# Kernel optimization log

Measured on AMD Instinct MI355X. Metric: run time of the kernel, lower is better.

The kernel has to match this reference:

```python
import jax, jax.numpy as jnp
import numpy as np

B, C, H, W = 4, 64, 256, 256
DS = 4        # ClusterLocalAtt downscale
CS = 2        # FastClusterAtt cluster_stride
NH = 4        # FastClusterAtt num_heads
G = 4         # OrthoConvClustering groups
N_NOISE = 8   # number of -1 (noise) labels; even and divisible by B


def _maxpool(x, k):
    b, c, h, w = x.shape
    return x.reshape(b, c, h // k, k, w // k, k).max(axis=(3, 5))


def _normalize(x, eps=1e-12):
    n = jnp.linalg.norm(x, axis=-1, keepdims=True)
    return x / jnp.maximum(n, eps)


def _feat_sim(cf, nf):
    # cf: (B,k,HW), nf: (B,n,HW) -> (B,k) mean cosine similarity over noise rows
    return jnp.einsum('bkl,bnl->bkn', _normalize(cf), _normalize(nf)).mean(-1)


def setup_inputs():
    key = jax.random.key(0)
    ks = jax.random.split(key, 12)
    x = jax.random.normal(ks[0], (B, C, H, W), jnp.float32)
    noise_idx = jnp.arange(N_NOISE, dtype=jnp.int32)
    labels = jax.random.randint(ks[1], (B * C,), 0, 12, dtype=jnp.int32)
    labels = labels.at[noise_idx].set(-1)
    inv = 1.0 / np.sqrt(C // G)
    return {
        'x': x, 'labels': labels, 'noise_idx': noise_idx,
        'qkv_w1': jax.random.normal(ks[2], (3 * C,), jnp.float32) * 0.5,
        'qkv_b1': jax.random.normal(ks[3], (3 * C,), jnp.float32) * 0.1,
        'up_k': jax.random.normal(ks[4], (C, DS, DS), jnp.float32) * 0.25,
        'up_b': jax.random.normal(ks[5], (C,), jnp.float32) * 0.1,
        'clu_w': jax.random.normal(ks[6], (G, C // G, C // G), jnp.float32) * inv,
        'clu_b': jnp.zeros((C,), jnp.float32),
        'qkv_w2': jax.random.normal(ks[7], (3 * C,), jnp.float32) * 0.5,
        'bais_w': jax.random.normal(ks[8], (C, C), jnp.float32) * (inv * 0.5),
        'bais_b': jax.random.normal(ks[9], (C,), jnp.float32) * 0.1,
    }


def reference(x, labels, noise_idx, qkv_w1, qkv_b1, up_k, up_b,
              clu_w, clu_b, qkv_w2, bais_w, bais_b):
    idx3 = jnp.arange(3 * C) // 3  # grouped 1x1 conv (groups=C): out ch j reads in ch j//3
    # ================= ClusterLocalAtt =================
    x_down = _maxpool(x, DS)                        # (B,C,Hd,Wd)
    Hd, Wd = H // DS, W // DS
    hw = Hd * Wd
    qkv = x_down[:, idx3] * qkv_w1[None, :, None, None] + qkv_b1[None, :, None, None]
    qkv = qkv.reshape(3 * B * C, hw)                # torch: reshape(1, 3*B*C, hw)
    q, k, v = jnp.split(qkv, 3, axis=0)             # each (B*C, hw) - batch/ch mixed, faithful
    valid = labels != -1
    allowed = (labels[:, None] == labels[None, :]) & valid[:, None] & valid[None, :]
    scores = q @ k.T                                # (BC, BC)
    attn = jax.nn.softmax(jnp.where(allowed, scores, -1e30), axis=-1)
    att = jnp.where(valid[:, None], attn @ v, 0.0)  # noise rows stay zero
    out = att.reshape(B, C, Hd, Wd)
    # depthwise ConvTranspose2d(kernel=DS, stride=DS): each input px -> DSxDS block
    up = jnp.einsum('bchw,cpq->bchpwq', out, up_k).reshape(B, C, H, W)
    up = up + up_b[None, :, None, None]
    noise = x.reshape(B * C, H * W)[noise_idx].reshape(B, N_NOISE // B, H * W)
    sim = _feat_sim(up.reshape(B, C, H * W), noise)[:, :, None, None]  # (B,C,1,1)
    out_clu = x + (up + (1.0 - sim) * x)
    # ================= FastClusterAtt =================
    xf = out_clu.reshape(B, G, C // G, H * W)
    xc = jnp.einsum('goi,bgil->bgol', clu_w, xf).reshape(B, C, H * W) + clu_b[None, :, None]
    x_ds = _maxpool(xc.reshape(B, C, H, W), CS)     # (B,C,Hs,Ws)
    Hs, Ws = H // CS, W // CS
    Ls = Hs * Ws
    qkv2 = (x_ds[:, idx3] * qkv_w2[None, :, None, None]).reshape(B, 3, NH, C // NH, Ls)
    qh, kh, vh = qkv2[:, 0], qkv2[:, 1], qkv2[:, 2]  # (B,NH,hd,Ls)
    sc = (qh * kh).sum(axis=2, keepdims=True) / np.sqrt(C // NH)  # (B,NH,1,Ls)
    a = jax.nn.softmax(sc, axis=-1)
    oh = (a * vh).sum(axis=-1).reshape(B, C)        # (B,C) global pooled heads
    # bilinear upsample of a spatially-constant map is the same constant -> skip interp
    ov = jnp.einsum('oc,bc->bo', bais_w, oh) + bais_b
    out_full = jnp.broadcast_to(ov[:, :, None, None], (B, C, H, W))
    sim2 = _feat_sim(out_full.reshape(B, C, H * W), noise)[:, :, None, None]
    WWT = jnp.einsum('goi,gpi->gop', clu_w, clu_w)
    I = jnp.eye(C // G, dtype=clu_w.dtype)
    ortho = 1.0 - jax.lax.stop_gradient(jnp.mean((WWT - I) ** 2))
    out2 = out_full * (1.0 - sim2) + ortho * out_clu
    return out_clu + out2
```

## Files before the change

### kernel.cpp

```cpp
#include <hip/hip_runtime.h>
#include <math.h>

#define WS_XD     0u
#define WS_S      1048576u
#define WS_GPART  1048832u
#define WS_COEF   2113792u
#define WS_CONST  2138368u
#define WS_ATT    2138624u
#define WS_FAC    3187200u
#define WS_XDS    3187456u
#define WS_ALPHA  7382016u
#define WS_BETA   7382272u
#define WS_NSTAT  7382273u
#define WS_P2     7382304u

__device__ __forceinline__ float bsum(float v, float* sd, int tid) {
    sd[tid] = v; __syncthreads();
    for (int off = 128; off > 0; off >>= 1) {
        if (tid < off) sd[tid] += sd[tid + off];
        __syncthreads();
    }
    float r = sd[0]; __syncthreads(); return r;
}
__device__ __forceinline__ float bmax(float v, float* sd, int tid) {
    sd[tid] = v; __syncthreads();
    for (int off = 128; off > 0; off >>= 1) {
        if (tid < off) sd[tid] = fmaxf(sd[tid], sd[tid + off]);
        __syncthreads();
    }
    float r = sd[0]; __syncthreads(); return r;
}

__global__ __launch_bounds__(256) void k_pool4(const float* __restrict__ x,
                                               const int* __restrict__ nidx,
                                               float* __restrict__ ws) {
    __shared__ float sd[256];
    int r = blockIdx.x, tid = threadIdx.x;
    const float4* xr = (const float4*)x + (size_t)r * 16384;
    float* xd = ws + WS_XD + (size_t)r * 4096;
    float sum = 0.f, s = 0.f, ss = 0.f;
    for (int it = 0; it < 16; ++it) {
        int o = it * 256 + tid;
        int h = o >> 6, w = o & 63;
        float m = -INFINITY;
        #pragma unroll
        for (int p = 0; p < 4; ++p) {
            float4 v = xr[(4 * h + p) * 64 + w];
            m = fmaxf(m, fmaxf(fmaxf(v.x, v.y), fmaxf(v.z, v.w)));
            s  += v.x + v.y + v.z + v.w;
            ss += v.x*v.x + v.y*v.y + v.z*v.z + v.w*v.w;
        }
        xd[o] = m; sum += m;
    }
    float st = bsum(sum, sd, tid);
    if (tid == 0) ws[WS_S + r] = st;
    bool isn = false;
    #pragma unroll
    for (int n = 0; n < 8; ++n) isn = isn || (nidx[n] == r);
    if (isn) {
        float ts = bsum(s, sd, tid);
        float tss = bsum(ss, sd, tid);
        if (tid == 0) {
            for (int n = 0; n < 8; ++n)
                if (nidx[n] == r) { ws[WS_NSTAT + n] = ts; ws[WS_NSTAT + 8 + n] = sqrtf(tss); }
        }
    }
}

__global__ __launch_bounds__(256) void k_gram(float* __restrict__ ws) {
    __shared__ __align__(16) float As[64][68];
    __shared__ __align__(16) float Bs[64][68];
    int tid = threadIdx.x, tx = tid & 15, ty = tid >> 4;
    int ra0 = blockIdx.y * 64, rb0 = 80 + blockIdx.x * 64, k0 = blockIdx.z * 64;
    const float4* xd4 = (const float4*)(ws + WS_XD);
    #pragma unroll
    for (int q = 0; q < 4; ++q) {
        int idx = q * 256 + tid;
        int row = idx >> 4, cf = idx & 15;
        float4 a = xd4[(size_t)(ra0 + row) * 1024 + (k0 >> 2) + cf];
        As[cf*4+0][row] = a.x; As[cf*4+1][row] = a.y; As[cf*4+2][row] = a.z; As[cf*4+3][row] = a.w;
        float4 b = xd4[(size_t)(rb0 + row) * 1024 + (k0 >> 2) + cf];
        Bs[cf*4+0][row] = b.x; Bs[cf*4+1][row] = b.y; Bs[cf*4+2][row] = b.z; Bs[cf*4+3][row] = b.w;
    }
    __syncthreads();
    float acc[4][4] = {};
    #pragma unroll 4
    for (int kk = 0; kk < 64; ++kk) {
        float4 a = *(const float4*)&As[kk][ty * 4];
        float4 b = *(const float4*)&Bs[kk][tx * 4];
        acc[0][0] += a.x*b.x; acc[0][1] += a.x*b.y; acc[0][2] += a.x*b.z; acc[0][3] += a.x*b.w;
        acc[1][0] += a.y*b.x; acc[1][1] += a.y*b.y; acc[1][2] += a.y*b.z; acc[1][3] += a.y*b.w;
        acc[2][0] += a.z*b.x; acc[2][1] += a.z*b.y; acc[2][2] += a.z*b.z; acc[2][3] += a.z*b.w;
        acc[3][0] += a.w*b.x; acc[3][1] += a.w*b.y; acc[3][2] += a.w*b.z; acc[3][3] += a.w*b.w;
    }
    float* gp = ws + WS_GPART + (size_t)blockIdx.z * 16384;
    #pragma unroll
    for (int i = 0; i < 4; ++i) {
        float4 o = make_float4(acc[i][0], acc[i][1], acc[i][2], acc[i][3]);
        *(float4*)&gp[(size_t)(ra0 + ty * 4 + i) * 128 + blockIdx.x * 64 + tx * 4] = o;
    }
}

__global__ __launch_bounds__(256) void k_attn1(const int* __restrict__ labels,
                                               const float* __restrict__ w1,
                                               const float* __restrict__ b1,
                                               float* __restrict__ ws) {
    __shared__ float sd[256];
    __shared__ float attn_s[256];
    __shared__ float grow[128];
    int i = blockIdx.x, tid = threadIdx.x;
    int labi = labels[i];
    bool validi = (labi != -1);
    int bi = (i >= 192) ? 1 : 0;
    int ji = i - bi * 192;
    int rq = bi * 64 + ji / 3;
    if (tid < 128) {
        const float* gp = ws + WS_GPART + (size_t)rq * 128 + tid;
        float acc = 0.f;
        #pragma unroll 8
        for (int p = 0; p < 64; ++p) acc += gp[(size_t)p * 16384];
        grow[tid] = acc;
    }
    __syncthreads();
    float wq = w1[ji], bq = b1[ji];
    int gk = 256 + tid;
    int bk = (gk >= 384) ? 2 : 1;
    int jk = gk - bk * 192;
    int rk = bk * 64 + jk / 3;
    float wk = w1[jk], bbk = b1[jk];
    int labj = labels[tid];
    bool allowed = validi && (labj == labi) && (labj != -1);
    float score = wq * wk * grow[rk - 80]
                + wq * bbk * ws[WS_S + rq]
                + wk * bq  * ws[WS_S + rk]
                + 4096.0f * bq * bbk;
    float sc = allowed ? score : -1e30f;
    float m = bmax(sc, sd, tid);
    float e = __expf(sc - m);
    float Z = bsum(e, sd, tid);
    float attn = validi ? (e / Z) : 0.0f;
    attn_s[tid] = attn;
    int gv = 512 + tid;
    int bv = (gv >= 576) ? 3 : 2;
    int jv = gv - bv * 192;
    float csum = bsum(attn * b1[jv], sd, tid);
    if (tid < 96) {
        float s = 0.0f;
        if (tid < 86) {
            int rv = 170 + tid;
            int lo, hi, jadd;
            if (rv < 192) { int c = rv - 128; lo = 3 * c; if (lo < 128) lo = 128; hi = 3 * c + 2; jadd = -128; }
            else          { int c = rv - 192; lo = 3 * c; hi = 3 * c + 2; jadd = 64; }
            for (int jj = lo; jj <= hi; ++jj) s += attn_s[jj + jadd] * w1[jj];
        }
        ws[WS_COEF + i * 96 + tid] = s;
    }
    if (tid == 0) ws[WS_CONST + i] = csum;
}

__global__ __launch_bounds__(256) void k_attmm(float* __restrict__ ws) {
    __shared__ __align__(16) float As[96][68];
    __shared__ __align__(16) float Bs[96][64];
    int tid = threadIdx.x, tx = tid & 15, ty = tid >> 4;
    int col0 = blockIdx.x * 64, row0 = blockIdx.y * 64;
    const float4* cf4 = (const float4*)(ws + WS_COEF);
    const float4* xd4 = (const float4*)(ws + WS_XD);
    #pragma unroll
    for (int q = 0; q < 6; ++q) {
        int f = q * 256 + tid;
        {
            int row = f / 24, c24 = f - row * 24;
            float4 v = cf4[(size_t)(row0 + row) * 24 + c24];
            As[c24*4+0][row] = v.x; As[c24*4+1][row] = v.y; As[c24*4+2][row] = v.z; As[c24*4+3][row] = v.w;
        }
        {
            int row = f >> 4, c16 = f & 15;
            float4 v = make_float4(0.f, 0.f, 0.f, 0.f);
            if (row < 86) v = xd4[(size_t)(170 + row) * 1024 + (col0 >> 2) + c16];
            *(float4*)&Bs[row][c16 * 4] = v;
        }
    }
    __syncthreads();
    float acc[4][4] = {};
    #pragma unroll 4
    for (int kk = 0; kk < 96; ++kk) {
        float4 a = *(const float4*)&As[kk][ty * 4];
        float4 b = *(const float4*)&Bs[kk][tx * 4];
        acc[0][0] += a.x*b.x; acc[0][1] += a.x*b.y; acc[0][2] += a.x*b.z; acc[0][3] += a.x*b.w;
        acc[1][0] += a.y*b.x; acc[1][1] += a.y*b.y; acc[1][2] += a.y*b.z; acc[1][3] += a.y*b.w;
        acc[2][0] += a.z*b.x; acc[2][1] += a.z*b.y; acc[2][2] += a.z*b.z; acc[2][3] += a.z*b.w;
        acc[3][0] += a.w*b.x; acc[3][1] += a.w*b.y; acc[3][2] += a.w*b.z; acc[3][3] += a.w*b.w;
    }
    float* att = ws + WS_ATT;
    #pragma unroll
    for (int i = 0; i < 4; ++i) {
        int row = row0 + ty * 4 + i;
        float cv = ws[WS_CONST + row];
        float4 o = make_float4(acc[i][0] + cv, acc[i][1] + cv, acc[i][2] + cv, acc[i][3] + cv);
        *(float4*)&att[(size_t)row * 4096 + col0 + tx * 4] = o;
    }
}

__global__ __launch_bounds__(256) void k_sim(const float* __restrict__ x,
                                             const int* __restrict__ nidx,
                                             const float* __restrict__ upk,
                                             const float* __restrict__ upb,
                                             float* __restrict__ ws) {
    __shared__ float sd[256];
    int r = blockIdx.x, tid = threadIdx.x;
    int b = r >> 6, c = r & 63;
    const float* att = ws + WS_ATT + (size_t)r * 4096;
    const float4* xn0 = (const float4*)x + (size_t)nidx[2 * b] * 16384;
    const float4* xn1 = (const float4*)x + (size_t)nidx[2 * b + 1] * 16384;
    const float4* k4p = (const float4*)upk + c * 4;
    float ub = upb[c];
    float4 kk0 = k4p[0], kk1 = k4p[1], kk2 = k4p[2], kk3 = k4p[3];
    float s2 = 0.f, d0 = 0.f, d1 = 0.f;
    for (int it = 0; it < 64; ++it) {
        int f = it * 256 + tid;
        int rowf = f >> 6, c4 = f & 63;
        float av = att[(rowf >> 2) * 64 + c4];
        int p = rowf & 3;
        float4 kv = (p == 0) ? kk0 : ((p == 1) ? kk1 : ((p == 2) ? kk2 : kk3));
        float4 a0 = xn0[f], a1 = xn1[f];
        float u;
        u = av * kv.x + ub; s2 += u * u; d0 += u * a0.x; d1 += u * a1.x;
        u = av * kv.y + ub; s2 += u * u; d0 += u * a0.y; d1 += u * a1.y;
        u = av * kv.z + ub; s2 += u * u; d0 += u * a0.z; d1 += u * a1.z;
        u = av * kv.w + ub; s2 += u * u; d0 += u * a0.w; d1 += u * a1.w;
    }
    s2 = bsum(s2, sd, tid);
    d0 = bsum(d0, sd, tid);
    d1 = bsum(d1, sd, tid);
    if (tid == 0) {
        float nup = fmaxf(sqrtf(s2), 1e-12f);
        float n0 = fmaxf(ws[WS_NSTAT + 8 + 2 * b], 1e-12f);
        float n1 = fmaxf(ws[WS_NSTAT + 8 + 2 * b + 1], 1e-12f);
        float sim = 0.5f * (d0 / (nup * n0) + d1 / (nup * n1));
        ws[WS_FAC + r] = 2.0f - sim;
    }
}

__global__ __launch_bounds__(128) void k_cluds(const float* __restrict__ x,
                                               const float* __restrict__ upk,
                                               const float* __restrict__ upb,
                                               const float* __restrict__ cw,
                                               const float* __restrict__ cb,
                                               float* __restrict__ ws) {
    __shared__ float wcl[256];
    __shared__ float kup[256];
    __shared__ float cbl[16], ubl[16], fcl[16];
    int h2 = blockIdx.x, g = blockIdx.y, b = blockIdx.z;
    int t = threadIdx.x;
    wcl[t] = cw[g * 256 + t];       wcl[t + 128] = cw[g * 256 + t + 128];
    kup[t] = upk[g * 256 + t];      kup[t + 128] = upk[g * 256 + t + 128];
    if (t < 16) {
        cbl[t] = cb[g * 16 + t];
        ubl[t] = upb[g * 16 + t];
        fcl[t] = ws[WS_FAC + b * 64 + g * 16 + t];
    }
    __syncthreads();
    int r0 = 2 * h2;
    int p0 = r0 & 3;
    int q0 = (2 * t) & 3;
    int h_att = h2 >> 1;
    int wa = t >> 1;
    const float* attb = ws + WS_ATT;
    float oc[16][4];
    #pragma unroll
    for (int i = 0; i < 16; ++i) {
        int ch = g * 16 + i;
        float av = attb[(size_t)(b * 64 + ch) * 4096 + h_att * 64 + wa];
        const float* xc = x + (size_t)(b * 64 + ch) * 65536;
        float2 x0 = *(const float2*)&xc[r0 * 256 + 2 * t];
        float2 x1 = *(const float2*)&xc[(r0 + 1) * 256 + 2 * t];
        float ub = ubl[i], fc = fcl[i];
        oc[i][0] = av * kup[i * 16 + p0 * 4 + q0]           + ub + fc * x0.x;
        oc[i][1] = av * kup[i * 16 + p0 * 4 + q0 + 1]       + ub + fc * x0.y;
        oc[i][2] = av * kup[i * 16 + (p0 + 1) * 4 + q0]     + ub + fc * x1.x;
        oc[i][3] = av * kup[i * 16 + (p0 + 1) * 4 + q0 + 1] + ub + fc * x1.y;
    }
    float* xds = ws + WS_XDS;
    #pragma unroll
    for (int o = 0; o < 16; ++o) {
        float cbv = cbl[o];
        float a0 = cbv, a1 = cbv, a2 = cbv, a3 = cbv;
        #pragma unroll
        for (int i = 0; i < 16; ++i) {
            float wv = wcl[o * 16 + i];
            a0 += wv * oc[i][0]; a1 += wv * oc[i][1];
            a2 += wv * oc[i][2]; a3 += wv * oc[i][3];
        }
        float m = fmaxf(fmaxf(a0, a1), fmaxf(a2, a3));
        xds[(size_t)((b * 64 + g * 16 + o) * 128 + h2) * 128 + t] = m;
    }
}

__global__ __launch_bounds__(256) void k_attn2a(const float* __restrict__ w2,
                                                float* __restrict__ ws) {
    __shared__ float wl2[192];
    __shared__ float ms[256], dsh[256];
    __shared__ float ns[256][17];
    int chunk = blockIdx.x, nh = blockIdx.y, b = blockIdx.z, tid = threadIdx.x;
    if (tid < 192) wl2[tid] = w2[tid];
    __syncthreads();
    const float4* X4 = (const float4*)(ws + WS_XDS + (size_t)b * 1048576);
    int li = chunk * 256 + tid;
    float4 sc = make_float4(0.f, 0.f, 0.f, 0.f);
    #pragma unroll
    for (int d = 0; d < 16; ++d) {
        int jq = nh * 16 + d, jk = 64 + nh * 16 + d;
        float4 q4 = X4[(size_t)(jq / 3) * 4096 + li];
        float4 k4 = X4[(size_t)(jk / 3) * 4096 + li];
        float wqk = wl2[jq] * wl2[jk] * 0.25f;
        sc.x += wqk * q4.x * k4.x; sc.y += wqk * q4.y * k4.y;
        sc.z += wqk * q4.z * k4.z; sc.w += wqk * q4.w * k4.w;
    }
    float m = fmaxf(fmaxf(sc.x, sc.y), fmaxf(sc.z, sc.w));
    float p0 = __expf(sc.x - m), p1 = __expf(sc.y - m), p2 = __expf(sc.z - m), p3 = __expf(sc.w - m);
    float den = p0 + p1 + p2 + p3;
    float num[16];
    #pragma unroll
    for (int d = 0; d < 16; ++d) {
        int jv = 128 + nh * 16 + d;
        float4 v4 = X4[(size_t)(jv / 3) * 4096 + li];
        num[d] = wl2[jv] * (p0 * v4.x + p1 * v4.y + p2 * v4.z + p3 * v4.w);
    }
    ms[tid] = m; dsh[tid] = den;
    #pragma unroll
    for (int d = 0; d < 16; ++d) ns[tid][d] = num[d];
    __syncthreads();
    for (int off = 128; off > 0; off >>= 1) {
        if (tid < off) {
            float ma = ms[tid], mb = ms[tid + off];
            float M = fmaxf(ma, mb);
            float ra = __expf(ma - M), rb = __expf(mb - M);
            dsh[tid] = dsh[tid] * ra + dsh[tid + off] * rb;
            #pragma unroll
            for (int d = 0; d < 16; ++d)
                ns[tid][d] = ns[tid][d] * ra + ns[tid + off][d] * rb;
            ms[tid] = M;
        }
        __syncthreads();
    }
    if (tid == 0) {
        float* p = ws + WS_P2 + ((size_t)(b * 4 + nh) * 16 + chunk) * 18;
        p[0] = ms[0]; p[1] = dsh[0];
        #pragma unroll
        for (int d = 0; d < 16; ++d) p[2 + d] = ns[0][d];
    }
}

__global__ __launch_bounds__(256) void k_tail(const float* __restrict__ bw,
                                              const float* __restrict__ bb,
                                              const float* __restrict__ cw,
                                              float* __restrict__ ws) {
    __shared__ float ohs[256], sd[256];
    int tid = threadIdx.x;
    int grp = tid >> 4;
    int j = tid & 15;
    const float* p = ws + WS_P2 + ((size_t)grp * 16 + j) * 18;
    float m = p[0], den = p[1], num[16];
    #pragma unroll
    for (int d = 0; d < 16; ++d) num[d] = p[2 + d];
    #pragma unroll
    for (int mask = 1; mask <= 8; mask <<= 1) {
        float mo = __shfl_xor(m, mask);
        float dn = __shfl_xor(den, mask);
        float M = fmaxf(m, mo);
        float ra = __expf(m - M), rb = __expf(mo - M);
        den = den * ra + dn * rb;
        #pragma unroll
        for (int d = 0; d < 16; ++d)
            num[d] = num[d] * ra + __shfl_xor(num[d], mask) * rb;
        m = M;
    }
    if (j == 0) {
        int b = grp >> 2, nh = grp & 3;
        #pragma unroll
        for (int d = 0; d < 16; ++d) ohs[b * 64 + nh * 16 + d] = num[d] / den;
    }
    __syncthreads();
    int b = tid >> 6, o = tid & 63;
    float s = bb[o];
    #pragma unroll 4
    for (int c2 = 0; c2 < 64; ++c2) s += bw[o * 64 + c2] * ohs[b * 64 + c2];
    float oacc = 0.f;
    for (int u = 0; u < 4; ++u) {
        int e = tid * 4 + u;
        int g = e >> 8, oo = (e >> 4) & 15, pp = e & 15;
        float ssv = 0.f;
        #pragma unroll
        for (int i = 0; i < 16; ++i) ssv += cw[g * 256 + oo * 16 + i] * cw[g * 256 + pp * 16 + i];
        float dd = ssv - ((oo == pp) ? 1.0f : 0.0f);
        oacc += dd * dd;
    }
    float tot = bsum(oacc, sd, tid);
    float nd = fmaxf(fabsf(s) * 256.0f, 1e-12f);
    float t0 = ws[WS_NSTAT + 2 * b], t1 = ws[WS_NSTAT + 2 * b + 1];
    float n0 = fmaxf(ws[WS_NSTAT + 8 + 2 * b], 1e-12f);
    float n1 = fmaxf(ws[WS_NSTAT + 8 + 2 * b + 1], 1e-12f);
    float sim2 = (s / nd) * 0.5f * (t0 / n0 + t1 / n1);
    ws[WS_ALPHA + tid] = (1.0f - sim2) * s;
    if (tid == 0) ws[WS_BETA] = 2.0f - tot / 1024.0f;
}

__global__ __launch_bounds__(256) void k_final(const float* __restrict__ x,
                                               const float* __restrict__ upk,
                                               const float* __restrict__ upb,
                                               const float* __restrict__ ws,
                                               float* __restrict__ out) {
    int idx = blockIdx.x * 256 + threadIdx.x;
    int r = idx >> 14;
    int rem = idx & 16383;
    int rowf = rem >> 6, c4 = rem & 63;
    int c = r & 63;
    float av = ws[WS_ATT + (size_t)r * 4096 + (rowf >> 2) * 64 + c4];
    int p = rowf & 3;
    float4 kv = ((const float4*)upk)[c * 4 + p];
    float ub = upb[c];
    float fac = ws[WS_FAC + r], al = ws[WS_ALPHA + r], be = ws[WS_BETA];
    float4 xv = ((const float4*)x)[idx];
    float4 o;
    o.x = be * (av * kv.x + ub + fac * xv.x) + al;
    o.y = be * (av * kv.y + ub + fac * xv.y) + al;
    o.z = be * (av * kv.z + ub + fac * xv.z) + al;
    o.w = be * (av * kv.w + ub + fac * xv.w) + al;
    ((float4*)out)[idx] = o;
}

extern "C" void kernel_launch(void* const* d_in, const int* in_sizes, int n_in,
                              void* d_out, int out_size, void* d_ws, size_t ws_size,
                              hipStream_t stream) {
    const float* x      = (const float*)d_in[0];
    const int*   labels = (const int*)d_in[1];
    const int*   nidx   = (const int*)d_in[2];
    const float* w1     = (const float*)d_in[3];
    const float* b1     = (const float*)d_in[4];
    const float* upk    = (const float*)d_in[5];
    const float* upb    = (const float*)d_in[6];
    const float* cw     = (const float*)d_in[7];
    const float* cb     = (const float*)d_in[8];
    const float* w2     = (const float*)d_in[9];
    const float* bw     = (const float*)d_in[10];
    const float* bb     = (const float*)d_in[11];
    float* ws  = (float*)d_ws;
    float* out = (float*)d_out;

    hipLaunchKernelGGL(k_pool4,  dim3(256),        dim3(256), 0, stream, x, nidx, ws);
    hipLaunchKernelGGL(k_gram,   dim3(2, 2, 64),   dim3(256), 0, stream, ws);
    hipLaunchKernelGGL(k_attn1,  dim3(256),        dim3(256), 0, stream, labels, w1, b1, ws);
    hipLaunchKernelGGL(k_attmm,  dim3(64, 4),      dim3(256), 0, stream, ws);
    hipLaunchKernelGGL(k_sim,    dim3(256),        dim3(256), 0, stream, x, nidx, upk, upb, ws);
    hipLaunchKernelGGL(k_cluds,  dim3(128, 4, 4),  dim3(128), 0, stream, x, upk, upb, cw, cb, ws);
    hipLaunchKernelGGL(k_attn2a, dim3(16, 4, 4),   dim3(256), 0, stream, w2, ws);
    hipLaunchKernelGGL(k_tail,   dim3(1),          dim3(256), 0, stream, bw, bb, cw, ws);
    hipLaunchKernelGGL(k_final,  dim3(16384),      dim3(256), 0, stream, x, upk, upb, ws, out);
}
```

Measured before the change: 107.9 us.

## Fuse attention tail into last-block reducer and trim pool/sim/cluds overheads

Merges the single-block tail kernel into the attention partial kernel. An atomic counter, zeroed by a memset, lets block 0 spin until all 256 blocks finish and then do the reduction, which removes one launch. The pool kernel becomes a template so non-noise rows skip the sum and sum-of-squares work, and k_sim does its three block reductions in one shared pass. k_cluds stages the attention row tile in shared memory instead of issuing scattered global loads per channel. The spin-wait depends on all blocks being co-resident or scheduled before block 0 stalls, and the memset adds an extra operation to the stream.

```diff
diff --git a/kernel.cpp b/kernel.cpp
--- a/kernel.cpp
+++ b/kernel.cpp
@@ -13,6 +13,7 @@
 #define WS_BETA   7382272u
 #define WS_NSTAT  7382273u
 #define WS_P2     7382304u
+#define WS_CNT    7386912u
 
 __device__ __forceinline__ float bsum(float v, float* sd, int tid) {
     sd[tid] = v; __syncthreads();
@@ -29,6 +30,27 @@
         __syncthreads();
     }
     float r = sd[0]; __syncthreads(); return r;
+}
+
+template <bool ISN>
+__device__ __forceinline__ void pool4_body(const float4* __restrict__ xr,
+                                           float* __restrict__ xd, int tid,
+                                           float& sum, float& s, float& ss) {
+    for (int it = 0; it < 16; ++it) {
+        int o = it * 256 + tid;
+        int h = o >> 6, w = o & 63;
+        float m = -INFINITY;
+        #pragma unroll
+        for (int p = 0; p < 4; ++p) {
+            float4 v = xr[(4 * h + p) * 64 + w];
+            m = fmaxf(m, fmaxf(fmaxf(v.x, v.y), fmaxf(v.z, v.w)));
+            if (ISN) {
+                s  += v.x + v.y + v.z + v.w;
+                ss += v.x*v.x + v.y*v.y + v.z*v.z + v.w*v.w;
+            }
+        }
+        xd[o] = m; sum += m;
+    }
 }
 
 __global__ __launch_bounds__(256) void k_pool4(const float* __restrict__ x,
@@ -38,25 +60,14 @@
     int r = blockIdx.x, tid = threadIdx.x;
     const float4* xr = (const float4*)x + (size_t)r * 16384;
     float* xd = ws + WS_XD + (size_t)r * 4096;
+    bool isn = false;
+    #pragma unroll
+    for (int n = 0; n < 8; ++n) isn = isn || (nidx[n] == r);
     float sum = 0.f, s = 0.f, ss = 0.f;
-    for (int it = 0; it < 16; ++it) {
-        int o = it * 256 + tid;
-        int h = o >> 6, w = o & 63;
-        float m = -INFINITY;
-        #pragma unroll
-        for (int p = 0; p < 4; ++p) {
-            float4 v = xr[(4 * h + p) * 64 + w];
-            m = fmaxf(m, fmaxf(fmaxf(v.x, v.y), fmaxf(v.z, v.w)));
-            s  += v.x + v.y + v.z + v.w;
-            ss += v.x*v.x + v.y*v.y + v.z*v.z + v.w*v.w;
-        }
-        xd[o] = m; sum += m;
-    }
+    if (isn) pool4_body<true>(xr, xd, tid, sum, s, ss);
+    else     pool4_body<false>(xr, xd, tid, sum, s, ss);
     float st = bsum(sum, sd, tid);
     if (tid == 0) ws[WS_S + r] = st;
-    bool isn = false;
-    #pragma unroll
-    for (int n = 0; n < 8; ++n) isn = isn || (nidx[n] == r);
     if (isn) {
         float ts = bsum(s, sd, tid);
         float tss = bsum(ss, sd, tid);
@@ -206,7 +217,7 @@
                                              const float* __restrict__ upk,
                                              const float* __restrict__ upb,
                                              float* __restrict__ ws) {
-    __shared__ float sd[256];
+    __shared__ float sd[768];
     int r = blockIdx.x, tid = threadIdx.x;
     int b = r >> 6, c = r & 63;
     const float* att = ws + WS_ATT + (size_t)r * 4096;
@@ -229,14 +240,21 @@
         u = av * kv.z + ub; s2 += u * u; d0 += u * a0.z; d1 += u * a1.z;
         u = av * kv.w + ub; s2 += u * u; d0 += u * a0.w; d1 += u * a1.w;
     }
-    s2 = bsum(s2, sd, tid);
-    d0 = bsum(d0, sd, tid);
-    d1 = bsum(d1, sd, tid);
+    sd[tid] = s2; sd[256 + tid] = d0; sd[512 + tid] = d1;
+    __syncthreads();
+    for (int off = 128; off > 0; off >>= 1) {
+        if (tid < off) {
+            sd[tid]       += sd[tid + off];
+            sd[256 + tid] += sd[256 + tid + off];
+            sd[512 + tid] += sd[512 + tid + off];
+        }
+        __syncthreads();
+    }
     if (tid == 0) {
-        float nup = fmaxf(sqrtf(s2), 1e-12f);
+        float nup = fmaxf(sqrtf(sd[0]), 1e-12f);
         float n0 = fmaxf(ws[WS_NSTAT + 8 + 2 * b], 1e-12f);
         float n1 = fmaxf(ws[WS_NSTAT + 8 + 2 * b + 1], 1e-12f);
-        float sim = 0.5f * (d0 / (nup * n0) + d1 / (nup * n1));
+        float sim = 0.5f * (sd[256] / (nup * n0) + sd[512] / (nup * n1));
         ws[WS_FAC + r] = 2.0f - sim;
     }
 }
@@ -250,6 +268,7 @@
     __shared__ float wcl[256];
     __shared__ float kup[256];
     __shared__ float cbl[16], ubl[16], fcl[16];
+    __shared__ float atile[16][64];
     int h2 = blockIdx.x, g = blockIdx.y, b = blockIdx.z;
     int t = threadIdx.x;
     wcl[t] = cw[g * 256 + t];       wcl[t + 128] = cw[g * 256 + t + 128];
@@ -259,18 +278,24 @@
         ubl[t] = upb[g * 16 + t];
         fcl[t] = ws[WS_FAC + b * 64 + g * 16 + t];
     }
+    int h_att = h2 >> 1;
+    {
+        int ch = t >> 3, cb4 = (t & 7) * 8;
+        const float4* arow = (const float4*)(ws + WS_ATT + (size_t)(b * 64 + g * 16 + ch) * 4096 + h_att * 64 + cb4);
+        float4 v0 = arow[0], v1 = arow[1];
+        *(float4*)&atile[ch][cb4] = v0;
+        *(float4*)&atile[ch][cb4 + 4] = v1;
+    }
     __syncthreads();
     int r0 = 2 * h2;
     int p0 = r0 & 3;
     int q0 = (2 * t) & 3;
-    int h_att = h2 >> 1;
     int wa = t >> 1;
-    const float* attb = ws + WS_ATT;
     float oc[16][4];
     #pragma unroll
     for (int i = 0; i < 16; ++i) {
         int ch = g * 16 + i;
-        float av = attb[(size_t)(b * 64 + ch) * 4096 + h_att * 64 + wa];
+        float av = atile[i][wa];
         const float* xc = x + (size_t)(b * 64 + ch) * 65536;
         float2 x0 = *(const float2*)&xc[r0 * 256 + 2 * t];
         float2 x1 = *(const float2*)&xc[(r0 + 1) * 256 + 2 * t];
@@ -296,12 +321,16 @@
     }
 }
 
-__global__ __launch_bounds__(256) void k_attn2a(const float* __restrict__ w2,
-                                                float* __restrict__ ws) {
+__global__ __launch_bounds__(256) void k_att2t(const float* __restrict__ w2,
+                                               const float* __restrict__ bw,
+                                               const float* __restrict__ bb,
+                                               const float* __restrict__ cw,
+                                               float* __restrict__ ws) {
     __shared__ float wl2[192];
     __shared__ float ms[256], dsh[256];
     __shared__ float ns[256][17];
-    int chunk = blockIdx.x, nh = blockIdx.y, b = blockIdx.z, tid = threadIdx.x;
+    int bid = blockIdx.x, tid = threadIdx.x;
+    int chunk = bid & 15, nh = (bid >> 4) & 3, b = bid >> 6;
     if (tid < 192) wl2[tid] = w2[tid];
     __syncthreads();
     const float4* X4 = (const float4*)(ws + WS_XDS + (size_t)b * 1048576);
@@ -349,42 +378,41 @@
         #pragma unroll
         for (int d = 0; d < 16; ++d) p[2 + d] = ns[0][d];
     }
-}
-
-__global__ __launch_bounds__(256) void k_tail(const float* __restrict__ bw,
-                                              const float* __restrict__ bb,
-                                              const float* __restrict__ cw,
-                                              float* __restrict__ ws) {
+    unsigned* cnt = (unsigned*)(ws + WS_CNT);
+    __syncthreads();
+    if (tid == 0) { __threadfence(); atomicAdd(cnt, 1u); }
+    if (bid != 0) return;
+    if (tid == 0) { while (atomicAdd(cnt, 0u) < 256u) {} __threadfence(); }
+    __syncthreads();
     __shared__ float ohs[256], sd[256];
-    int tid = threadIdx.x;
     int grp = tid >> 4;
     int j = tid & 15;
     const float* p = ws + WS_P2 + ((size_t)grp * 16 + j) * 18;
-    float m = p[0], den = p[1], num[16];
-    #pragma unroll
-    for (int d = 0; d < 16; ++d) num[d] = p[2 + d];
+    float mm = p[0], dden = p[1], nnum[16];
+    #pragma unroll
+    for (int d = 0; d < 16; ++d) nnum[d] = p[2 + d];
     #pragma unroll
     for (int mask = 1; mask <= 8; mask <<= 1) {
-        float mo = __shfl_xor(m, mask);
-        float dn = __shfl_xor(den, mask);
-        float M = fmaxf(m, mo);
-        float ra = __expf(m - M), rb = __expf(mo - M);
-        den = den * ra + dn * rb;
+        float mo = __shfl_xor(mm, mask);
+        float dn = __shfl_xor(dden, mask);
+        float M = fmaxf(mm, mo);
+        float ra = __expf(mm - M), rb = __expf(mo - M);
+        dden = dden * ra + dn * rb;
         #pragma unroll
         for (int d = 0; d < 16; ++d)
-            num[d] = num[d] * ra + __shfl_xor(num[d], mask) * rb;
-        m = M;
+            nnum[d] = nnum[d] * ra + __shfl_xor(nnum[d], mask) * rb;
+        mm = M;
     }
     if (j == 0) {
-        int b = grp >> 2, nh = grp & 3;
-        #pragma unroll
-        for (int d = 0; d < 16; ++d) ohs[b * 64 + nh * 16 + d] = num[d] / den;
-    }
-    __syncthreads();
-    int b = tid >> 6, o = tid & 63;
+        int bb2 = grp >> 2, nh2 = grp & 3;
+        #pragma unroll
+        for (int d = 0; d < 16; ++d) ohs[bb2 * 64 + nh2 * 16 + d] = nnum[d] / dden;
+    }
+    __syncthreads();
+    int b2 = tid >> 6, o = tid & 63;
     float s = bb[o];
     #pragma unroll 4
-    for (int c2 = 0; c2 < 64; ++c2) s += bw[o * 64 + c2] * ohs[b * 64 + c2];
+    for (int c2 = 0; c2 < 64; ++c2) s += bw[o * 64 + c2] * ohs[b2 * 64 + c2];
     float oacc = 0.f;
     for (int u = 0; u < 4; ++u) {
         int e = tid * 4 + u;
@@ -397,9 +425,9 @@
     }
     float tot = bsum(oacc, sd, tid);
     float nd = fmaxf(fabsf(s) * 256.0f, 1e-12f);
-    float t0 = ws[WS_NSTAT + 2 * b], t1 = ws[WS_NSTAT + 2 * b + 1];
-    float n0 = fmaxf(ws[WS_NSTAT + 8 + 2 * b], 1e-12f);
-    float n1 = fmaxf(ws[WS_NSTAT + 8 + 2 * b + 1], 1e-12f);
+    float t0 = ws[WS_NSTAT + 2 * b2], t1 = ws[WS_NSTAT + 2 * b2 + 1];
+    float n0 = fmaxf(ws[WS_NSTAT + 8 + 2 * b2], 1e-12f);
+    float n1 = fmaxf(ws[WS_NSTAT + 8 + 2 * b2 + 1], 1e-12f);
     float sim2 = (s / nd) * 0.5f * (t0 / n0 + t1 / n1);
     ws[WS_ALPHA + tid] = (1.0f - sim2) * s;
     if (tid == 0) ws[WS_BETA] = 2.0f - tot / 1024.0f;
@@ -447,13 +475,14 @@
     float* ws  = (float*)d_ws;
     float* out = (float*)d_out;
 
+    hipMemsetAsync((char*)d_ws + WS_CNT * sizeof(float), 0, sizeof(unsigned), stream);
+
     hipLaunchKernelGGL(k_pool4,  dim3(256),        dim3(256), 0, stream, x, nidx, ws);
     hipLaunchKernelGGL(k_gram,   dim3(2, 2, 64),   dim3(256), 0, stream, ws);
     hipLaunchKernelGGL(k_attn1,  dim3(256),        dim3(256), 0, stream, labels, w1, b1, ws);
     hipLaunchKernelGGL(k_attmm,  dim3(64, 4),      dim3(256), 0, stream, ws);
     hipLaunchKernelGGL(k_sim,    dim3(256),        dim3(256), 0, stream, x, nidx, upk, upb, ws);
     hipLaunchKernelGGL(k_cluds,  dim3(128, 4, 4),  dim3(128), 0, stream, x, upk, upb, cw, cb, ws);
-    hipLaunchKernelGGL(k_attn2a, dim3(16, 4, 4),   dim3(256), 0, stream, w2, ws);
-    hipLaunchKernelGGL(k_tail,   dim3(1),          dim3(256), 0, stream, bw, bb, cw, ws);
+    hipLaunchKernelGGL(k_att2t,  dim3(256),        dim3(256), 0, stream, w2, bw, bb, cw, ws);
     hipLaunchKernelGGL(k_final,  dim3(16384),      dim3(256), 0, stream, x, upk, upb, ws, out);
 }
```

After: 121.2 us. 12.3% more time.
